# Kernel optimization log

Measured on AMD Instinct MI355X. Metric: run time of the kernel, lower is better.

Reference implementation:

```python
import jax, jax.numpy as jnp
import numpy as np

N_NODES = 50000
N_EDGES = 1600000
IN_CH = 128
OUT_CH = 16
K_HOPS = 2


def setup_inputs() -> dict:
    key = jax.random.key(0)
    k1, k2, k3, k4 = jax.random.split(key, 4)
    x = jax.random.normal(k1, (N_NODES, IN_CH), dtype=jnp.float32)
    W = jax.random.normal(k2, (OUT_CH, IN_CH), dtype=jnp.float32) * 0.05
    edge_weight = jax.random.uniform(k3, (N_EDGES,), dtype=jnp.float32)
    edge_index = jax.random.randint(k4, (2, N_EDGES), 0, N_NODES, dtype=jnp.int64)
    return {"x": x, "W": W, "edge_weight": edge_weight,
            "edge_index": edge_index, "K": K_HOPS}


def reference(x, W, edge_weight, edge_index, K):
    N = x.shape[0]
    # --- gcn_norm with add_self_loops=True (fill_value = 1.0) ---
    loops = jnp.arange(N, dtype=edge_index.dtype)
    row = jnp.concatenate([edge_index[0], loops])  # source nodes
    col = jnp.concatenate([edge_index[1], loops])  # target nodes
    w = jnp.concatenate([edge_weight, jnp.ones((N,), dtype=x.dtype)])
    deg = jax.ops.segment_sum(w, col, num_segments=N)  # degree at targets
    dinv = jnp.where(deg > 0, jax.lax.rsqrt(deg), 0.0)
    norm = dinv[row] * w * dinv[col]  # [E+N]

    # --- K-hop propagation: h <- A_hat @ h (gather-scale-scatter) ---
    def hop(h, _):
        msgs = norm[:, None] * h[row]               # [E+N, F] gather + scale
        h = jax.ops.segment_sum(msgs, col, num_segments=N)  # scatter-add
        return h, None

    h, _ = jax.lax.scan(hop, x, None, length=K)

    # --- linear projection (bias=False) then log_softmax over classes ---
    logits = h @ W.T  # [N, out_channels]
    return jax.nn.log_softmax(logits, axis=1)
```

## Files before the change

### kernel.cpp

```cpp
#include <hip/hip_runtime.h>
#include <hip/hip_fp16.h>
#include <math.h>

#define IN_CH 128
#define OUT_CH 16
#define B 256
#define CH_H 2048
#define CH_P 4096
#define LSH 6
#define LNODES 64
#define MAXNL 1024
#define MAXGH 2048

__device__ __forceinline__ unsigned short f2h(float f) {
    __half h = __float2half(f);
    unsigned short u;
    __builtin_memcpy(&u, &h, 2);
    return u;
}
__device__ __forceinline__ float h2f(unsigned short u) {
    __half h;
    __builtin_memcpy(&h, &u, 2);
    return __half2float(h);
}

__device__ __forceinline__ void scan_nl(const unsigned* __restrict__ vals, unsigned* dst,
                                        unsigned* sums, int NL) {
    int tid = threadIdx.x;
    int b0 = tid * 4;
    unsigned v[4]; unsigned loc = 0;
#pragma unroll
    for (int q = 0; q < 4; ++q) { int i = b0 + q; v[q] = (i < NL) ? vals[i] : 0u; loc += v[q]; }
    sums[tid] = loc;
    __syncthreads();
    for (int off = 1; off < B; off <<= 1) {
        unsigned a = (tid >= off) ? sums[tid - off] : 0u;
        __syncthreads();
        sums[tid] += a;
        __syncthreads();
    }
    unsigned run = sums[tid] - loc;
#pragma unroll
    for (int q = 0; q < 4; ++q) { int i = b0 + q; if (i < NL) dst[i] = run; run += v[q]; }
    __syncthreads();
}

__global__ void __launch_bounds__(B) k_hist(const int* __restrict__ col,
                                            unsigned* __restrict__ bh, int E, int NL) {
    __shared__ unsigned hc[MAXNL];
    int tid = threadIdx.x;
    for (int i = tid; i < NL; i += B) hc[i] = 0u;
    __syncthreads();
    int base = blockIdx.x * CH_H;
    int end = base + CH_H < E ? base + CH_H : E;
    for (int e = base + tid; e < end; e += B)
        atomicAdd(&hc[col[e] >> LSH], 1u);
    __syncthreads();
    unsigned* out = bh + (size_t)blockIdx.x * NL;
    for (int i = tid; i < NL; i += B) out[i] = hc[i];
}

__global__ void __launch_bounds__(B) k_colscan(unsigned* __restrict__ bh,
                                               unsigned* __restrict__ tot, int G, int NL) {
    int j = blockIdx.x;
    __shared__ unsigned s[B];
    int tid = threadIdx.x;
    unsigned carry = 0;
    for (int g0 = 0; g0 < G; g0 += B) {
        __syncthreads();
        int g = g0 + tid;
        unsigned v = (g < G) ? bh[(size_t)g * NL + j] : 0u;
        s[tid] = v;
        __syncthreads();
        for (int off = 1; off < B; off <<= 1) {
            unsigned add = (tid >= off) ? s[tid - off] : 0u;
            __syncthreads();
            s[tid] += add;
            __syncthreads();
        }
        if (g < G) bh[(size_t)g * NL + j] = carry + s[tid] - v;
        carry += s[B - 1];
    }
    if (tid == 0) tot[j] = carry;
}

__global__ void __launch_bounds__(B)
k_place(const int* __restrict__ row, const int* __restrict__ col, const float* __restrict__ ew,
        const unsigned* __restrict__ bh, const unsigned* __restrict__ tot,
        uint2* __restrict__ rec, int E, int NL, int G_H, int F) {
    __shared__ uint2 srec[CH_P];
    __shared__ unsigned short slf[CH_P];
    __shared__ unsigned obase[MAXNL];
    __shared__ unsigned lscan[MAXNL];
    __shared__ unsigned lctr[MAXNL];
    __shared__ unsigned sums[B];
    int tid = threadIdx.x;
    int c = blockIdx.x;
    int base = c * CH_P;
    int end = base + CH_P < E ? base + CH_P : E;
    int cnt = end - base;
    int g0 = c * F;

    scan_nl(tot, lscan, sums, NL);
    {
        const unsigned* r0 = bh + (size_t)g0 * NL;
        bool has2 = (g0 + F) < G_H;
        const unsigned* r2 = bh + (size_t)(g0 + F) * NL;
        for (int i = tid; i < NL; i += B) {
            unsigned b0 = r0[i];
            unsigned bn = has2 ? r2[i] : tot[i];
            obase[i] = lscan[i] + b0;
            lctr[i] = bn - b0;
        }
    }
    __syncthreads();
    scan_nl(lctr, lscan, sums, NL);
    for (int i = tid; i < NL; i += B) lctr[i] = lscan[i];
    __syncthreads();
    for (int j = tid; j < cnt; j += B) {
        int e = base + j;
        int cc = col[e];
        int lf = cc >> LSH;
        unsigned pos = atomicAdd(&lctr[lf], 1u);
        srec[pos] = make_uint2(((unsigned)row[e] << 6) | (unsigned)(cc & (LNODES - 1)),
                               __float_as_uint(ew[e]));
        slf[pos] = (unsigned short)lf;
    }
    __syncthreads();
    for (int j = tid; j < cnt; j += B) {
        int lf = slf[j];
        unsigned outp = obase[lf] + ((unsigned)j - lscan[lf]);
        rec[outp] = srec[j];
    }
}

__global__ void __launch_bounds__(B)
k_sort2proj(const uint2* __restrict__ rec, const unsigned* __restrict__ tot,
            const float* __restrict__ x, const float* __restrict__ W,
            unsigned* __restrict__ rec2, unsigned* __restrict__ nptr,
            float* __restrict__ dinv, float* __restrict__ g0, int N, int NL) {
    __shared__ unsigned sums[B];
    __shared__ unsigned gbase[MAXNL];
    __shared__ unsigned hist[LNODES];
    __shared__ unsigned start[LNODES];
    __shared__ unsigned nstart[LNODES];
    __shared__ float dloc[LNODES];
    __shared__ float sW[OUT_CH * 132];
    int l = blockIdx.x, tid = threadIdx.x;

    for (int i = tid; i < OUT_CH * IN_CH; i += B) {
        sW[(i >> 7) * 132 + (i & 127)] = W[i];
    }
    scan_nl(tot, gbase, sums, NL);
    int seg = (int)gbase[l];
    int cnt = (int)tot[l];
    if (tid < LNODES) hist[tid] = 0u;
    __syncthreads();
    for (int j = seg + tid; j < seg + cnt; j += B)
        atomicAdd(&hist[rec[j].x & (LNODES - 1)], 1u);
    __syncthreads();
    if (tid < LNODES) {
        unsigned v = hist[tid];
        unsigned sum = v;
        for (int off = 1; off < LNODES; off <<= 1) {
            unsigned o = __shfl_up(sum, off, 64);
            if (tid >= off) sum += o;
        }
        unsigned st = (unsigned)seg + sum - v;
        start[tid] = st;
        nstart[tid] = st;
        int n = l * LNODES + tid;
        if (n < N) nptr[n] = st;
    }
    if (l == NL - 1 && tid == 0) nptr[N] = (unsigned)(seg + cnt);
    __syncthreads();
    for (int j = seg + tid; j < seg + cnt; j += B) {
        uint2 u = rec[j];
        int cc = (int)(u.x & (LNODES - 1));
        unsigned pos = atomicAdd(&start[cc], 1u);
        rec2[pos] = ((u.x >> 6) << 16) | (unsigned)f2h(__uint_as_float(u.y));
    }
    __syncthreads();
    {
        int o = tid & 15;
        for (int nl = tid >> 4; nl < LNODES; nl += 16) {
            int j0 = (int)nstart[nl];
            int j1 = (nl + 1 < LNODES) ? (int)nstart[nl + 1] : seg + cnt;
            float wsum = 0.f;
            for (int j = j0 + o; j < j1; j += 16) wsum += h2f((unsigned short)rec2[j]);
#pragma unroll
            for (int off = 1; off < 16; off <<= 1) wsum += __shfl_xor(wsum, off, 16);
            if (o == 0) {
                float dn = rsqrtf(1.0f + wsum);
                dloc[nl] = dn;
                int n = l * LNODES + nl;
                if (n < N) dinv[n] = dn;
            }
        }
    }
    __syncthreads();
    int o = tid & 15;
    for (int nl = tid >> 4; nl < LNODES; nl += 16) {
        int n = l * LNODES + nl;
        if (n >= N) break;
        const float* xr = x + (size_t)n * IN_CH;
        const float* wr = sW + o * 132;
        float acc = 0.0f;
#pragma unroll
        for (int k = 0; k < IN_CH; k += 4) {
            float4 xv = *reinterpret_cast<const float4*>(xr + k);
            float4 wv = *reinterpret_cast<const float4*>(wr + k);
            acc += xv.x * wv.x + xv.y * wv.y + xv.z * wv.z + xv.w * wv.w;
        }
        g0[(size_t)n * OUT_CH + o] = dloc[nl] * acc;
    }
}

template <bool FINAL>
__global__ void __launch_bounds__(B)
k_hop(const unsigned* __restrict__ rec2, const unsigned* __restrict__ nptr,
      const float* __restrict__ dinv, const float* __restrict__ gin,
      float* __restrict__ out, int N) {
    int t = blockIdx.x * B + threadIdx.x;
    int n = t >> 4, ch = t & 15;
    if (n >= N) return;
    int j0 = (int)nptr[n], j1 = (int)nptr[n + 1];
    float acc = 0.f;
    int j = j0;
    for (; j + 3 < j1; j += 4) {
        unsigned u0 = rec2[j], u1 = rec2[j + 1], u2 = rec2[j + 2], u3 = rec2[j + 3];
        acc += h2f((unsigned short)u0) * gin[(size_t)(u0 >> 16) * OUT_CH + ch]
             + h2f((unsigned short)u1) * gin[(size_t)(u1 >> 16) * OUT_CH + ch]
             + h2f((unsigned short)u2) * gin[(size_t)(u2 >> 16) * OUT_CH + ch]
             + h2f((unsigned short)u3) * gin[(size_t)(u3 >> 16) * OUT_CH + ch];
    }
    for (; j < j1; ++j) {
        unsigned u = rec2[j];
        acc += h2f((unsigned short)u) * gin[(size_t)(u >> 16) * OUT_CH + ch];
    }
    float d = dinv[n];
    float s = gin[(size_t)n * OUT_CH + ch] + acc;
    if (!FINAL) {
        out[(size_t)n * OUT_CH + ch] = d * d * s;
    } else {
        float v = d * s;
        float m = v;
#pragma unroll
        for (int off = 1; off < 16; off <<= 1) m = fmaxf(m, __shfl_xor(m, off, 16));
        float se = expf(v - m);
#pragma unroll
        for (int off = 1; off < 16; off <<= 1) se += __shfl_xor(se, off, 16);
        out[(size_t)n * OUT_CH + ch] = v - m - logf(se);
    }
}


__global__ void fb_deginit(float* deg, int N) {
    int i = blockIdx.x * blockDim.x + threadIdx.x;
    if (i < N) deg[i] = 1.0f;
}
__global__ void fb_deg(const int* __restrict__ col, const float* __restrict__ ew,
                       float* deg, int E) {
    int e = blockIdx.x * blockDim.x + threadIdx.x;
    if (e < E) atomicAdd(&deg[col[e]], ew[e]);
}
__global__ void fb_dinv(const float* __restrict__ deg, float* dinv, int N) {
    int i = blockIdx.x * blockDim.x + threadIdx.x;
    if (i < N) dinv[i] = rsqrtf(deg[i]);
}
__global__ void fb_proj(const float* __restrict__ x, const float* __restrict__ W,
                        float* __restrict__ y, int N) {
    __shared__ float sW[OUT_CH * 132];
    for (int i = threadIdx.x; i < OUT_CH * IN_CH; i += blockDim.x) {
        sW[(i >> 7) * 132 + (i & 127)] = W[i];
    }
    __syncthreads();
    int t = threadIdx.x;
    int n = blockIdx.x * 16 + (t >> 4);
    int o = t & 15;
    if (n >= N) return;
    const float* xr = x + (size_t)n * IN_CH;
    const float* wr = sW + o * 132;
    float acc = 0.0f;
#pragma unroll
    for (int k = 0; k < IN_CH; k += 4) {
        float4 xv = *reinterpret_cast<const float4*>(xr + k);
        float4 wv = *reinterpret_cast<const float4*>(wr + k);
        acc += xv.x * wv.x + xv.y * wv.y + xv.z * wv.z + xv.w * wv.w;
    }
    y[(size_t)n * OUT_CH + o] = acc;
}
__global__ void fb_selfinit(const float* __restrict__ hin, const float* __restrict__ dinv,
                            float* __restrict__ hout, int N) {
    int idx = blockIdx.x * blockDim.x + threadIdx.x;
    if (idx < N * OUT_CH) {
        float d = dinv[idx >> 4];
        hout[idx] = d * d * hin[idx];
    }
}
__global__ void fb_scat(const int* __restrict__ row, const int* __restrict__ col,
                        const float* __restrict__ ew, const float* __restrict__ dinv,
                        const float* __restrict__ hin, float* __restrict__ hout, int E) {
    long long idx = (long long)blockIdx.x * blockDim.x + threadIdx.x;
    int e = (int)(idx >> 4);
    int c = (int)(idx & 15);
    if (e >= E) return;
    int r = row[e], cl = col[e];
    float nv = dinv[r] * ew[e] * dinv[cl];
    atomicAdd(&hout[(size_t)cl * OUT_CH + c], nv * hin[(size_t)r * OUT_CH + c]);
}
__global__ void fb_lsm(const float* __restrict__ h, float* __restrict__ out, int N) {
    int n = blockIdx.x * blockDim.x + threadIdx.x;
    if (n >= N) return;
    const float* hr = h + (size_t)n * OUT_CH;
    float v[OUT_CH];
#pragma unroll
    for (int i = 0; i < OUT_CH; i++) v[i] = hr[i];
    float m = v[0];
#pragma unroll
    for (int i = 1; i < OUT_CH; i++) m = fmaxf(m, v[i]);
    float s = 0.0f;
#pragma unroll
    for (int i = 0; i < OUT_CH; i++) s += expf(v[i] - m);
    float lse = m + logf(s);
    float* orow = out + (size_t)n * OUT_CH;
#pragma unroll
    for (int i = 0; i < OUT_CH; i++) orow[i] = v[i] - lse;
}


extern "C" void kernel_launch(void* const* d_in, const int* in_sizes, int n_in,
                              void* d_out, int out_size, void* d_ws, size_t ws_size,
                              hipStream_t stream) {
    const float* x  = (const float*)d_in[0];
    const float* W  = (const float*)d_in[1];
    const float* ew = (const float*)d_in[2];
    const int*   ei = (const int*)d_in[3];

    int N = in_sizes[0] / IN_CH;
    int E = in_sizes[2];
    const int* row = ei;
    const int* col = ei + E;

    auto al = [](size_t v) { return (v + 255) & ~(size_t)255; };
    size_t N16 = (size_t)N * OUT_CH;

    int NL  = (N + LNODES - 1) >> LSH;
    int G_H = (E + CH_H - 1) / CH_H;
    int G_P = (E + CH_P - 1) / CH_P;
    int F   = CH_P / CH_H;
    int gH  = (int)((N16 + B - 1) / B);

    size_t o_rec  = 0;
    size_t o_rec2 = o_rec  + al((size_t)E * 8);
    size_t o_bh   = o_rec2 + al((size_t)E * 4);
    size_t o_tot  = o_bh   + al((size_t)G_H * NL * 4);
    size_t o_nptr = o_tot  + al((size_t)NL * 4);
    size_t o_dinv = o_nptr + al((size_t)(N + 1) * 4);
    size_t o_g0   = o_dinv + al((size_t)N * 4);
    size_t o_g1   = o_g0   + al(N16 * 4);
    size_t need   = o_g1   + al(N16 * 4);

    bool shape_ok = (NL <= MAXNL && G_H <= MAXGH && N <= 65536 &&
                     (G_P * F) <= G_H + F);

    char* ws = (char*)d_ws;

    if (shape_ok && need <= ws_size) {
        uint2*    rec  = (uint2*)(ws + o_rec);
        unsigned* rec2 = (unsigned*)(ws + o_rec2);
        unsigned* bh   = (unsigned*)(ws + o_bh);
        unsigned* tot  = (unsigned*)(ws + o_tot);
        unsigned* nptr = (unsigned*)(ws + o_nptr);
        float*    dinv = (float*)(ws + o_dinv);
        float*    g0   = (float*)(ws + o_g0);
        float*    g1   = (float*)(ws + o_g1);

        k_hist     <<<G_H, B, 0, stream>>>(col, bh, E, NL);
        k_colscan  <<<NL,  B, 0, stream>>>(bh, tot, G_H, NL);
        k_place    <<<G_P, B, 0, stream>>>(row, col, ew, bh, tot, rec, E, NL, G_H, F);
        k_sort2proj<<<NL,  B, 0, stream>>>(rec, tot, x, W, rec2, nptr, dinv, g0, N, NL);
        k_hop<false><<<gH, B, 0, stream>>>(rec2, nptr, dinv, g0, g1, N);
        k_hop<true ><<<gH, B, 0, stream>>>(rec2, nptr, dinv, g1, (float*)d_out, N);
    } else {
        size_t f_deg  = 0;
        size_t f_dinv = f_deg  + al((size_t)N * 4);
        size_t f_h0   = f_dinv + al((size_t)N * 4);
        size_t f_h1   = f_h0   + al(N16 * 4);
        float* deg  = (float*)(ws + f_deg);
        float* dinv = (float*)(ws + f_dinv);
        float* h0   = (float*)(ws + f_h0);
        float* h1   = (float*)(ws + f_h1);

        int gN   = (N + B - 1) / B;
        int gE   = (E + B - 1) / B;
        int gN16 = (N * OUT_CH + B - 1) / B;
        long long scat = (long long)E * OUT_CH;
        int gScat = (int)((scat + B - 1) / B);

        fb_deginit<<<gN, B, 0, stream>>>(deg, N);
        fb_deg<<<gE, B, 0, stream>>>(col, ew, deg, E);
        fb_dinv<<<gN, B, 0, stream>>>(deg, dinv, N);
        fb_proj<<<(N + 15) / 16, B, 0, stream>>>(x, W, h0, N);
        float* hin = h0; float* hout = h1;
        for (int k = 0; k < 2; k++) {
            fb_selfinit<<<gN16, B, 0, stream>>>(hin, dinv, hout, N);
            fb_scat<<<gScat, B, 0, stream>>>(row, col, ew, dinv, hin, hout, E);
            float* t = hin; hin = hout; hout = t;
        }
        fb_lsm<<<gN, B, 0, stream>>>(hin, (float*)d_out, N);
    }
}
```

Baseline: 113.2 us.

## Move projection into histogram kernel, apply source dinv in first hop, per-wave sort counters

The x@W^T projection moves out of the sort kernel into extra blocks of the histogram launch, so it runs alongside the histogram work and the projected features are stored unscaled. The first hop now multiplies each edge weight by the source node's dinv on the fly, which costs an extra gather per edge. The sort kernel uses four per-wavefront counter sets to reduce LDS atomic contention. These changes shorten the serial sort kernel in exchange for more random reads in the first hop.

```diff
diff --git a/kernel.cpp b/kernel.cpp
--- a/kernel.cpp
+++ b/kernel.cpp
@@ -9,6 +9,7 @@
 #define CH_P 4096
 #define LSH 6
 #define LNODES 64
+#define NW 4
 #define MAXNL 1024
 #define MAXGH 2048
 
@@ -45,19 +46,41 @@
     __syncthreads();
 }
 
-__global__ void __launch_bounds__(B) k_hist(const int* __restrict__ col,
-                                            unsigned* __restrict__ bh, int E, int NL) {
+__global__ void __launch_bounds__(B)
+k_histproj(const int* __restrict__ col, unsigned* __restrict__ bh,
+           const float* __restrict__ x, const float* __restrict__ W,
+           float* __restrict__ p, int E, int N, int NL, int G_H) {
     __shared__ unsigned hc[MAXNL];
+    __shared__ float sW[OUT_CH * 132];
     int tid = threadIdx.x;
-    for (int i = tid; i < NL; i += B) hc[i] = 0u;
-    __syncthreads();
-    int base = blockIdx.x * CH_H;
-    int end = base + CH_H < E ? base + CH_H : E;
-    for (int e = base + tid; e < end; e += B)
-        atomicAdd(&hc[col[e] >> LSH], 1u);
-    __syncthreads();
-    unsigned* out = bh + (size_t)blockIdx.x * NL;
-    for (int i = tid; i < NL; i += B) out[i] = hc[i];
+    if ((int)blockIdx.x < G_H) {
+        for (int i = tid; i < NL; i += B) hc[i] = 0u;
+        __syncthreads();
+        int base = blockIdx.x * CH_H;
+        int end = base + CH_H < E ? base + CH_H : E;
+        for (int e = base + tid; e < end; e += B)
+            atomicAdd(&hc[col[e] >> LSH], 1u);
+        __syncthreads();
+        unsigned* out = bh + (size_t)blockIdx.x * NL;
+        for (int i = tid; i < NL; i += B) out[i] = hc[i];
+    } else {
+        for (int i = tid; i < OUT_CH * IN_CH; i += B)
+            sW[(i >> 7) * 132 + (i & 127)] = W[i];
+        __syncthreads();
+        int n = ((int)blockIdx.x - G_H) * 16 + (tid >> 4);
+        int o = tid & 15;
+        if (n >= N) return;
+        const float* xr = x + (size_t)n * IN_CH;
+        const float* wr = sW + o * 132;
+        float acc = 0.0f;
+#pragma unroll
+        for (int k = 0; k < IN_CH; k += 4) {
+            float4 xv = *reinterpret_cast<const float4*>(xr + k);
+            float4 wv = *reinterpret_cast<const float4*>(wr + k);
+            acc += xv.x * wv.x + xv.y * wv.y + xv.z * wv.z + xv.w * wv.w;
+        }
+        p[(size_t)n * OUT_CH + o] = acc;
+    }
 }
 
 __global__ void __launch_bounds__(B) k_colscan(unsigned* __restrict__ bh,
@@ -135,40 +158,39 @@
 }
 
 __global__ void __launch_bounds__(B)
-k_sort2proj(const uint2* __restrict__ rec, const unsigned* __restrict__ tot,
-            const float* __restrict__ x, const float* __restrict__ W,
-            unsigned* __restrict__ rec2, unsigned* __restrict__ nptr,
-            float* __restrict__ dinv, float* __restrict__ g0, int N, int NL) {
+k_sort2(const uint2* __restrict__ rec, const unsigned* __restrict__ tot,
+        unsigned* __restrict__ rec2, unsigned* __restrict__ nptr,
+        float* __restrict__ dinv, int N, int NL) {
     __shared__ unsigned sums[B];
     __shared__ unsigned gbase[MAXNL];
-    __shared__ unsigned hist[LNODES];
-    __shared__ unsigned start[LNODES];
+    __shared__ unsigned cnt4[NW * LNODES];
+    __shared__ unsigned start4[NW * LNODES];
     __shared__ unsigned nstart[LNODES];
-    __shared__ float dloc[LNODES];
-    __shared__ float sW[OUT_CH * 132];
     int l = blockIdx.x, tid = threadIdx.x;
-
-    for (int i = tid; i < OUT_CH * IN_CH; i += B) {
-        sW[(i >> 7) * 132 + (i & 127)] = W[i];
-    }
+    int w = tid >> 6;
     scan_nl(tot, gbase, sums, NL);
     int seg = (int)gbase[l];
     int cnt = (int)tot[l];
-    if (tid < LNODES) hist[tid] = 0u;
+    for (int i = tid; i < NW * LNODES; i += B) cnt4[i] = 0u;
     __syncthreads();
     for (int j = seg + tid; j < seg + cnt; j += B)
-        atomicAdd(&hist[rec[j].x & (LNODES - 1)], 1u);
+        atomicAdd(&cnt4[w * LNODES + (rec[j].x & (LNODES - 1))], 1u);
     __syncthreads();
     if (tid < LNODES) {
-        unsigned v = hist[tid];
-        unsigned sum = v;
+        unsigned c0 = cnt4[tid], c1 = cnt4[LNODES + tid];
+        unsigned c2 = cnt4[2 * LNODES + tid], c3 = cnt4[3 * LNODES + tid];
+        unsigned totn = c0 + c1 + c2 + c3;
+        unsigned sum = totn;
         for (int off = 1; off < LNODES; off <<= 1) {
             unsigned o = __shfl_up(sum, off, 64);
             if (tid >= off) sum += o;
         }
-        unsigned st = (unsigned)seg + sum - v;
-        start[tid] = st;
+        unsigned st = (unsigned)seg + sum - totn;
         nstart[tid] = st;
+        start4[tid] = st;
+        start4[LNODES + tid] = st + c0;
+        start4[2 * LNODES + tid] = st + c0 + c1;
+        start4[3 * LNODES + tid] = st + c0 + c1 + c2;
         int n = l * LNODES + tid;
         if (n < N) nptr[n] = st;
     }
@@ -177,46 +199,26 @@
     for (int j = seg + tid; j < seg + cnt; j += B) {
         uint2 u = rec[j];
         int cc = (int)(u.x & (LNODES - 1));
-        unsigned pos = atomicAdd(&start[cc], 1u);
+        unsigned pos = atomicAdd(&start4[w * LNODES + cc], 1u);
         rec2[pos] = ((u.x >> 6) << 16) | (unsigned)f2h(__uint_as_float(u.y));
-    }
-    __syncthreads();
-    {
-        int o = tid & 15;
-        for (int nl = tid >> 4; nl < LNODES; nl += 16) {
-            int j0 = (int)nstart[nl];
-            int j1 = (nl + 1 < LNODES) ? (int)nstart[nl + 1] : seg + cnt;
-            float wsum = 0.f;
-            for (int j = j0 + o; j < j1; j += 16) wsum += h2f((unsigned short)rec2[j]);
-#pragma unroll
-            for (int off = 1; off < 16; off <<= 1) wsum += __shfl_xor(wsum, off, 16);
-            if (o == 0) {
-                float dn = rsqrtf(1.0f + wsum);
-                dloc[nl] = dn;
-                int n = l * LNODES + nl;
-                if (n < N) dinv[n] = dn;
-            }
-        }
     }
     __syncthreads();
     int o = tid & 15;
     for (int nl = tid >> 4; nl < LNODES; nl += 16) {
-        int n = l * LNODES + nl;
-        if (n >= N) break;
-        const float* xr = x + (size_t)n * IN_CH;
-        const float* wr = sW + o * 132;
-        float acc = 0.0f;
-#pragma unroll
-        for (int k = 0; k < IN_CH; k += 4) {
-            float4 xv = *reinterpret_cast<const float4*>(xr + k);
-            float4 wv = *reinterpret_cast<const float4*>(wr + k);
-            acc += xv.x * wv.x + xv.y * wv.y + xv.z * wv.z + xv.w * wv.w;
-        }
-        g0[(size_t)n * OUT_CH + o] = dloc[nl] * acc;
-    }
-}
-
-template <bool FINAL>
+        int j0 = (int)nstart[nl];
+        int j1 = (nl + 1 < LNODES) ? (int)nstart[nl + 1] : seg + cnt;
+        float wsum = 0.f;
+        for (int j = j0 + o; j < j1; j += 16) wsum += h2f((unsigned short)rec2[j]);
+#pragma unroll
+        for (int off = 1; off < 16; off <<= 1) wsum += __shfl_xor(wsum, off, 16);
+        if (o == 0) {
+            int n = l * LNODES + nl;
+            if (n < N) dinv[n] = rsqrtf(1.0f + wsum);
+        }
+    }
+}
+
+template <bool FIRST>
 __global__ void __launch_bounds__(B)
 k_hop(const unsigned* __restrict__ rec2, const unsigned* __restrict__ nptr,
       const float* __restrict__ dinv, const float* __restrict__ gin,
@@ -229,21 +231,28 @@
     int j = j0;
     for (; j + 3 < j1; j += 4) {
         unsigned u0 = rec2[j], u1 = rec2[j + 1], u2 = rec2[j + 2], u3 = rec2[j + 3];
-        acc += h2f((unsigned short)u0) * gin[(size_t)(u0 >> 16) * OUT_CH + ch]
-             + h2f((unsigned short)u1) * gin[(size_t)(u1 >> 16) * OUT_CH + ch]
-             + h2f((unsigned short)u2) * gin[(size_t)(u2 >> 16) * OUT_CH + ch]
-             + h2f((unsigned short)u3) * gin[(size_t)(u3 >> 16) * OUT_CH + ch];
+        float w0 = h2f((unsigned short)u0), w1 = h2f((unsigned short)u1);
+        float w2 = h2f((unsigned short)u2), w3 = h2f((unsigned short)u3);
+        if (FIRST) {
+            w0 *= dinv[u0 >> 16]; w1 *= dinv[u1 >> 16];
+            w2 *= dinv[u2 >> 16]; w3 *= dinv[u3 >> 16];
+        }
+        acc += w0 * gin[(size_t)(u0 >> 16) * OUT_CH + ch]
+             + w1 * gin[(size_t)(u1 >> 16) * OUT_CH + ch]
+             + w2 * gin[(size_t)(u2 >> 16) * OUT_CH + ch]
+             + w3 * gin[(size_t)(u3 >> 16) * OUT_CH + ch];
     }
     for (; j < j1; ++j) {
         unsigned u = rec2[j];
-        acc += h2f((unsigned short)u) * gin[(size_t)(u >> 16) * OUT_CH + ch];
+        float ww = h2f((unsigned short)u);
+        if (FIRST) ww *= dinv[u >> 16];
+        acc += ww * gin[(size_t)(u >> 16) * OUT_CH + ch];
     }
     float d = dinv[n];
-    float s = gin[(size_t)n * OUT_CH + ch] + acc;
-    if (!FINAL) {
-        out[(size_t)n * OUT_CH + ch] = d * d * s;
+    if (FIRST) {
+        out[(size_t)n * OUT_CH + ch] = d * d * (d * gin[(size_t)n * OUT_CH + ch] + acc);
     } else {
-        float v = d * s;
+        float v = d * (gin[(size_t)n * OUT_CH + ch] + acc);
         float m = v;
 #pragma unroll
         for (int off = 1; off < 16; off <<= 1) m = fmaxf(m, __shfl_xor(m, off, 16));
@@ -349,6 +358,7 @@
     int G_H = (E + CH_H - 1) / CH_H;
     int G_P = (E + CH_P - 1) / CH_P;
     int F   = CH_P / CH_H;
+    int NP16 = (N + 15) / 16;
     int gH  = (int)((N16 + B - 1) / B);
 
     size_t o_rec  = 0;
@@ -357,8 +367,8 @@
     size_t o_tot  = o_bh   + al((size_t)G_H * NL * 4);
     size_t o_nptr = o_tot  + al((size_t)NL * 4);
     size_t o_dinv = o_nptr + al((size_t)(N + 1) * 4);
-    size_t o_g0   = o_dinv + al((size_t)N * 4);
-    size_t o_g1   = o_g0   + al(N16 * 4);
+    size_t o_p    = o_dinv + al((size_t)N * 4);
+    size_t o_g1   = o_p    + al(N16 * 4);
     size_t need   = o_g1   + al(N16 * 4);
 
     bool shape_ok = (NL <= MAXNL && G_H <= MAXGH && N <= 65536 &&
@@ -373,15 +383,15 @@
         unsigned* tot  = (unsigned*)(ws + o_tot);
         unsigned* nptr = (unsigned*)(ws + o_nptr);
         float*    dinv = (float*)(ws + o_dinv);
-        float*    g0   = (float*)(ws + o_g0);
+        float*    p    = (float*)(ws + o_p);
         float*    g1   = (float*)(ws + o_g1);
 
-        k_hist     <<<G_H, B, 0, stream>>>(col, bh, E, NL);
+        k_histproj <<<G_H + NP16, B, 0, stream>>>(col, bh, x, W, p, E, N, NL, G_H);
         k_colscan  <<<NL,  B, 0, stream>>>(bh, tot, G_H, NL);
         k_place    <<<G_P, B, 0, stream>>>(row, col, ew, bh, tot, rec, E, NL, G_H, F);
-        k_sort2proj<<<NL,  B, 0, stream>>>(rec, tot, x, W, rec2, nptr, dinv, g0, N, NL);
-        k_hop<false><<<gH, B, 0, stream>>>(rec2, nptr, dinv, g0, g1, N);
-        k_hop<true ><<<gH, B, 0, stream>>>(rec2, nptr, dinv, g1, (float*)d_out, N);
+        k_sort2    <<<NL,  B, 0, stream>>>(rec, tot, rec2, nptr, dinv, N, NL);
+        k_hop<true ><<<gH, B, 0, stream>>>(rec2, nptr, dinv, p, g1, N);
+        k_hop<false><<<gH, B, 0, stream>>>(rec2, nptr, dinv, g1, (float*)d_out, N);
     } else {
         size_t f_deg  = 0;
         size_t f_dinv = f_deg  + al((size_t)N * 4);
```

Result: no change. 113.3 us (median of 2 runs) (+0.1%).
